# Performance work log

Hardware: AMD Instinct MI355X
Metric: run time of the kernel (lower is better)

The kernel has to match this reference:

```python
import jax, jax.numpy as jnp
import numpy as np

H, D_IN, D_Q, D_V = 8, 16, 32, 32
N = M = 4096


def setup_inputs() -> dict:
    key = jax.random.key(0)
    ks = jax.random.split(key, 12)
    s_in = 1.0 / np.sqrt(D_IN)
    s_fc = 1.0 / np.sqrt(H * D_V)
    return {
        "x": jax.random.normal(ks[0], (N, D_IN), jnp.float32),
        "y": jax.random.normal(ks[1], (M, D_IN), jnp.float32),
        # per-head stacked weights: [H, D_IN, D_Q/ D_V]
        "Wq": jax.random.uniform(ks[2], (H, D_IN, D_Q), jnp.float32, -s_in, s_in),
        "bq": jax.random.uniform(ks[3], (H, D_Q), jnp.float32, -s_in, s_in),
        "Wk": jax.random.uniform(ks[4], (H, D_IN, D_Q), jnp.float32, -s_in, s_in),
        "bk": jax.random.uniform(ks[5], (H, D_Q), jnp.float32, -s_in, s_in),
        "Wv": jax.random.uniform(ks[6], (H, D_IN, D_V), jnp.float32, -s_in, s_in),
        "bv": jax.random.uniform(ks[7], (H, D_V), jnp.float32, -s_in, s_in),
        "Wo": jax.random.uniform(ks[8], (H * D_V, D_IN), jnp.float32, -s_fc, s_fc),
        "bo": jax.random.uniform(ks[9], (D_IN,), jnp.float32, -s_fc, s_fc),
    }


def reference(x, y, Wq, bq, Wk, bk, Wv, bv, Wo, bo):
    # batched per-head projections (fuses the 8 tiny Linears of the torch loop)
    q = jnp.einsum("nd,hdq->hnq", x, Wq) + bq[:, None, :]   # [H, N, D_Q]
    k = jnp.einsum("md,hdq->hmq", y, Wk) + bk[:, None, :]   # [H, M, D_Q]
    v = jnp.einsum("md,hdv->hmv", y, Wv) + bv[:, None, :]   # [H, M, D_V]
    scores = jnp.einsum("hnq,hmq->hnm", q, k) / jnp.sqrt(jnp.float32(D_Q))
    attn = jax.nn.softmax(scores, axis=-1)                  # [H, N, M]
    heads = jnp.einsum("hnm,hmv->hnv", attn, v)             # [H, N, D_V]
    # torch.cat(head_outputs, dim=-1): head h occupies columns [h*D_V:(h+1)*D_V]
    concat = jnp.transpose(heads, (1, 0, 2)).reshape(x.shape[0], H * D_V)
    return concat @ Wo + bo                                  # [N, D_IN]
```

## Files before the change

### kernel.cpp

```cpp
#include <hip/hip_runtime.h>
#include <hip/hip_bf16.h>

typedef __attribute__((ext_vector_type(8))) short bf16x8;
typedef __attribute__((ext_vector_type(4))) float f32x4;
typedef unsigned short u16;
typedef unsigned int u32;

#define NH 8
#define NN 4096
#define MM 4096

__device__ __forceinline__ u16 f2bf(float f) {
  u32 b = __float_as_uint(f);
  b += 0x7FFFu + ((b >> 16) & 1u);
  return (u16)(b >> 16);
}

__device__ __forceinline__ u32 pack_rnu(float a, float b) {
  u32 ua = __float_as_uint(a) + 0x8000u;
  u32 ub = __float_as_uint(b) + 0x8000u;
#if __has_builtin(__builtin_amdgcn_perm)
  return __builtin_amdgcn_perm(ub, ua, 0x07060302u);
#else
  return (ua >> 16) | (ub & 0xFFFF0000u);
#endif
}

#if __has_builtin(__builtin_amdgcn_exp2f)
__device__ __forceinline__ float exp2_fast(float x) { return __builtin_amdgcn_exp2f(x); }
#else
__device__ __forceinline__ float exp2_fast(float x) { return __expf(x * 0.69314718055994531f); }
#endif

__global__ __launch_bounds__(256) void proj_kernel(
    const float* __restrict__ x, const float* __restrict__ y,
    const float* __restrict__ Wq, const float* __restrict__ bq,
    const float* __restrict__ Wk, const float* __restrict__ bk,
    const float* __restrict__ Wv, const float* __restrict__ bv,
    u16* __restrict__ qs, u16* __restrict__ ks, u16* __restrict__ vT)
{
  __shared__ u16 sv[256][33];
  const int bid = blockIdx.x;
  const int tid = threadIdx.x;
  if (bid < 256) {
    int idx = bid * 256 + tid;
    int t = idx >> 15;
    int h = (idx >> 12) & 7;
    int row = idx & 4095;
    const float* src = (t ? y : x) + row * 16;
    const float* W = (t ? Wk : Wq) + (h << 9);
    const float* b = (t ? bk : bq) + (h << 5);
    const float scale = t ? 1.0f : 0.25503635116465163f;
    float4 r4[4];
#pragma unroll
    for (int i = 0; i < 4; ++i) r4[i] = ((const float4*)src)[i];
    const float* r = (const float*)r4;
    u16* out = (t ? ks : qs) + (idx & 32767) * 32;
#pragma unroll
    for (int j = 0; j < 32; ++j) {
      float a = b[j];
#pragma unroll
      for (int i = 0; i < 16; ++i) a = fmaf(r[i], W[i * 32 + j], a);
      out[j] = f2bf(a * scale);
    }
  } else {
    int vb = bid - 256;
    int h = vb >> 4;
    int kb = (vb & 15) << 8;
    const float* src = y + (kb + tid) * 16;
    const float* W = Wv + (h << 9);
    const float* b = bv + (h << 5);
    float4 r4[4];
#pragma unroll
    for (int i = 0; i < 4; ++i) r4[i] = ((const float4*)src)[i];
    const float* r = (const float*)r4;
#pragma unroll
    for (int j = 0; j < 32; ++j) {
      float a = b[j];
#pragma unroll
      for (int i = 0; i < 16; ++i) a = fmaf(r[i], W[i * 32 + j], a);
      sv[tid][j] = f2bf(a);
    }
    __syncthreads();
    int dv = tid >> 3;
    int c = (tid & 7) << 5;
    u16* dst = vT + (((h << 5) + dv) << 12) + kb + c;
#pragma unroll
    for (int q = 0; q < 4; ++q) {
      uint4 w;
      w.x = (u32)sv[c + 4 * q + 0][dv]      | ((u32)sv[c + 4 * q + 1][dv] << 16);
      w.y = (u32)sv[c + 4 * q + 2][dv]      | ((u32)sv[c + 4 * q + 3][dv] << 16);
      w.z = (u32)sv[c + 16 + 4 * q + 0][dv] | ((u32)sv[c + 16 + 4 * q + 1][dv] << 16);
      w.w = (u32)sv[c + 16 + 4 * q + 2][dv] | ((u32)sv[c + 16 + 4 * q + 3][dv] << 16);
      *(uint4*)(dst + q * 8) = w;
    }
  }
}

#define KST 40
#define VST 72
#define VSZ (32 * VST)

__global__ __launch_bounds__(256) void flash_kernel(
    const u16* __restrict__ qs, const u16* __restrict__ ksrc,
    const u16* __restrict__ vT, float* __restrict__ accP,
    float* __restrict__ lsumP)
{
  __shared__ u16 sK[128 * KST];
  __shared__ u16 sVT[2 * VSZ];
  const int h = blockIdx.y;
  const int qt = blockIdx.x;
  const int z = blockIdx.z;
  const int nIter = (MM / 128) / gridDim.z;
  const int kb0 = z * (MM / gridDim.z);
  const int tid = threadIdx.x;
  const int wv = tid >> 6;
  const int lane = tid & 63;
  const int d = lane & 15;
  const int g = lane >> 4;
  const int qrowA = (qt << 7) + (wv << 5) + d;
  const int qrowB = qrowA + 16;

  union U4 { uint4 q; bf16x8 v; };
  U4 qfA, qfB;
  qfA.q = *(const uint4*)(qs + (((h << 12) + qrowA) << 5) + (g << 3));
  qfB.q = *(const uint4*)(qs + (((h << 12) + qrowB) << 5) + (g << 3));

  float lsA = 0.f, lsB = 0.f;
  f32x4 accA0 = {0.f, 0.f, 0.f, 0.f}, accA1 = {0.f, 0.f, 0.f, 0.f};
  f32x4 accB0 = {0.f, 0.f, 0.f, 0.f}, accB1 = {0.f, 0.f, 0.f, 0.f};
  const f32x4 zero = {0.f, 0.f, 0.f, 0.f};

  const u16* gK = ksrc + (h << 17) + (kb0 << 5) + ((tid >> 1) << 5) + ((tid & 1) << 4);
  const u16* gV = vT + (((h << 5) + (tid >> 3)) << 12) + kb0 + ((tid & 7) << 4);
  u16* wK = sK + (tid >> 1) * KST + ((tid & 1) << 4);
  u16* wV = sVT + ((tid & 7) >> 2) * VSZ + (tid >> 3) * VST + ((tid & 7) & 3) * 16;

  {
    uint4 a = *(const uint4*)gK, b = *(const uint4*)(gK + 8);
    uint4 c = *(const uint4*)gV, e = *(const uint4*)(gV + 8);
    *(uint4*)wK = a; *(uint4*)(wK + 8) = b;
    *(uint4*)wV = c; *(uint4*)(wV + 8) = e;
  }
  __syncthreads();

  auto compute = [&](const u16* kb, const u16* vb) {
    U4 kf[4];
#pragma unroll
    for (int t = 0; t < 4; ++t)
      kf[t].q = *(const uint4*)(kb + (t * 16 + d) * KST + (g << 3));

    union { u32 w[4]; bf16x8 v; } pbA0, pbA1, pbB0, pbB1;
    {
      f32x4 s0, s1, s2, s3;
      s0 = __builtin_amdgcn_mfma_f32_16x16x32_bf16(kf[0].v, qfA.v, zero, 0, 0, 0);
      s1 = __builtin_amdgcn_mfma_f32_16x16x32_bf16(kf[1].v, qfA.v, zero, 0, 0, 0);
      s2 = __builtin_amdgcn_mfma_f32_16x16x32_bf16(kf[2].v, qfA.v, zero, 0, 0, 0);
      s3 = __builtin_amdgcn_mfma_f32_16x16x32_bf16(kf[3].v, qfA.v, zero, 0, 0, 0);
      float e[16];
      e[0]=exp2_fast(s0.x); e[1]=exp2_fast(s0.y); e[2]=exp2_fast(s0.z); e[3]=exp2_fast(s0.w);
      e[4]=exp2_fast(s1.x); e[5]=exp2_fast(s1.y); e[6]=exp2_fast(s1.z); e[7]=exp2_fast(s1.w);
      e[8]=exp2_fast(s2.x); e[9]=exp2_fast(s2.y); e[10]=exp2_fast(s2.z); e[11]=exp2_fast(s2.w);
      e[12]=exp2_fast(s3.x); e[13]=exp2_fast(s3.y); e[14]=exp2_fast(s3.z); e[15]=exp2_fast(s3.w);
      lsA += ((e[0]+e[1])+(e[2]+e[3])) + ((e[4]+e[5])+(e[6]+e[7]))
           + ((e[8]+e[9])+(e[10]+e[11])) + ((e[12]+e[13])+(e[14]+e[15]));
      pbA0.w[0] = pack_rnu(e[0], e[1]);   pbA0.w[1] = pack_rnu(e[2], e[3]);
      pbA0.w[2] = pack_rnu(e[4], e[5]);   pbA0.w[3] = pack_rnu(e[6], e[7]);
      pbA1.w[0] = pack_rnu(e[8], e[9]);   pbA1.w[1] = pack_rnu(e[10], e[11]);
      pbA1.w[2] = pack_rnu(e[12], e[13]); pbA1.w[3] = pack_rnu(e[14], e[15]);
    }
    {
      f32x4 s0, s1, s2, s3;
      s0 = __builtin_amdgcn_mfma_f32_16x16x32_bf16(kf[0].v, qfB.v, zero, 0, 0, 0);
      s1 = __builtin_amdgcn_mfma_f32_16x16x32_bf16(kf[1].v, qfB.v, zero, 0, 0, 0);
      s2 = __builtin_amdgcn_mfma_f32_16x16x32_bf16(kf[2].v, qfB.v, zero, 0, 0, 0);
      s3 = __builtin_amdgcn_mfma_f32_16x16x32_bf16(kf[3].v, qfB.v, zero, 0, 0, 0);
      float e[16];
      e[0]=exp2_fast(s0.x); e[1]=exp2_fast(s0.y); e[2]=exp2_fast(s0.z); e[3]=exp2_fast(s0.w);
      e[4]=exp2_fast(s1.x); e[5]=exp2_fast(s1.y); e[6]=exp2_fast(s1.z); e[7]=exp2_fast(s1.w);
      e[8]=exp2_fast(s2.x); e[9]=exp2_fast(s2.y); e[10]=exp2_fast(s2.z); e[11]=exp2_fast(s2.w);
      e[12]=exp2_fast(s3.x); e[13]=exp2_fast(s3.y); e[14]=exp2_fast(s3.z); e[15]=exp2_fast(s3.w);
      lsB += ((e[0]+e[1])+(e[2]+e[3])) + ((e[4]+e[5])+(e[6]+e[7]))
           + ((e[8]+e[9])+(e[10]+e[11])) + ((e[12]+e[13])+(e[14]+e[15]));
      pbB0.w[0] = pack_rnu(e[0], e[1]);   pbB0.w[1] = pack_rnu(e[2], e[3]);
      pbB0.w[2] = pack_rnu(e[4], e[5]);   pbB0.w[3] = pack_rnu(e[6], e[7]);
      pbB1.w[0] = pack_rnu(e[8], e[9]);   pbB1.w[1] = pack_rnu(e[10], e[11]);
      pbB1.w[2] = pack_rnu(e[12], e[13]); pbB1.w[3] = pack_rnu(e[14], e[15]);
    }
    U4 vf0, vf1, vf2, vf3;
    const u16* vp = vb + d * VST;
    vf0.q = *(const uint4*)(vp + (g << 3));
    vf1.q = *(const uint4*)(vp + 32 + (g << 3));
    vp += 16 * VST;
    vf2.q = *(const uint4*)(vp + (g << 3));
    vf3.q = *(const uint4*)(vp + 32 + (g << 3));
    accA0 = __builtin_amdgcn_mfma_f32_16x16x32_bf16(vf0.v, pbA0.v, accA0, 0, 0, 0);
    accA0 = __builtin_amdgcn_mfma_f32_16x16x32_bf16(vf1.v, pbA1.v, accA0, 0, 0, 0);
    accA1 = __builtin_amdgcn_mfma_f32_16x16x32_bf16(vf2.v, pbA0.v, accA1, 0, 0, 0);
    accA1 = __builtin_amdgcn_mfma_f32_16x16x32_bf16(vf3.v, pbA1.v, accA1, 0, 0, 0);
    accB0 = __builtin_amdgcn_mfma_f32_16x16x32_bf16(vf0.v, pbB0.v, accB0, 0, 0, 0);
    accB0 = __builtin_amdgcn_mfma_f32_16x16x32_bf16(vf1.v, pbB1.v, accB0, 0, 0, 0);
    accB1 = __builtin_amdgcn_mfma_f32_16x16x32_bf16(vf2.v, pbB0.v, accB1, 0, 0, 0);
    accB1 = __builtin_amdgcn_mfma_f32_16x16x32_bf16(vf3.v, pbB1.v, accB1, 0, 0, 0);
  };

#pragma unroll 1
  for (int it = 0; it < nIter; ++it) {
    uint4 a, b, c, e;
    if (it < nIter - 1) {
      gK += 4096; gV += 128;
      a = *(const uint4*)gK; b = *(const uint4*)(gK + 8);
      c = *(const uint4*)gV; e = *(const uint4*)(gV + 8);
    }
    compute(sK, sVT);
    compute(sK + 64 * KST, sVT + VSZ);
    __syncthreads();
    if (it < nIter - 1) {
      *(uint4*)wK = a; *(uint4*)(wK + 8) = b;
      *(uint4*)wV = c; *(uint4*)(wV + 8) = e;
      __syncthreads();
    }
  }

  lsA += __shfl_xor(lsA, 16);
  lsA += __shfl_xor(lsA, 32);
  lsB += __shfl_xor(lsB, 16);
  lsB += __shfl_xor(lsB, 32);
  if (g == 0) {
    lsumP[((z * NH + h) << 12) + qrowA] = lsA;
    lsumP[((z * NH + h) << 12) + qrowB] = lsB;
  }
  float* cpA = accP + z * (NN * 256) + (qrowA << 8) + (h << 5) + (g << 2);
  *(float4*)cpA        = make_float4(accA0.x, accA0.y, accA0.z, accA0.w);
  *(float4*)(cpA + 16) = make_float4(accA1.x, accA1.y, accA1.z, accA1.w);
  float* cpB = accP + z * (NN * 256) + (qrowB << 8) + (h << 5) + (g << 2);
  *(float4*)cpB        = make_float4(accB0.x, accB0.y, accB0.z, accB0.w);
  *(float4*)(cpB + 16) = make_float4(accB1.x, accB1.y, accB1.z, accB1.w);
}

__global__ __launch_bounds__(256) void combine_kernel(
    const float* __restrict__ accP, const float* __restrict__ lsumP,
    float* __restrict__ concat, int S)
{
  int idx = blockIdx.x * 256 + threadIdx.x;
  int n = idx >> 8;
  int h = (idx & 255) >> 5;
  float o = 0.f, l = 0.f;
  for (int s = 0; s < S; ++s) {
    o += accP[s * (NN * 256) + idx];
    l += lsumP[((s * NH + h) << 12) + n];
  }
  concat[idx] = o / l;
}

__global__ __launch_bounds__(256) void out_gemm_kernel(
    const float* __restrict__ concat, const float* __restrict__ Wo,
    const float* __restrict__ bo, float* __restrict__ out)
{
  __shared__ float sWo[4096];
  int tid = threadIdx.x;
  for (int i = tid; i < 4096; i += 256) sWo[i] = Wo[i];
  __syncthreads();
  int idx = blockIdx.x * 256 + tid;
  int n = idx >> 4;
  int c = idx & 15;
  const float4* crow = (const float4*)(concat + (n << 8));
  float a = bo[c];
#pragma unroll 4
  for (int i4 = 0; i4 < 64; ++i4) {
    float4 cv = crow[i4];
    a = fmaf(cv.x, sWo[(i4 * 4 + 0) * 16 + c], a);
    a = fmaf(cv.y, sWo[(i4 * 4 + 1) * 16 + c], a);
    a = fmaf(cv.z, sWo[(i4 * 4 + 2) * 16 + c], a);
    a = fmaf(cv.w, sWo[(i4 * 4 + 3) * 16 + c], a);
  }
  out[idx] = a;
}

extern "C" void kernel_launch(void* const* d_in, const int* in_sizes, int n_in,
                              void* d_out, int out_size, void* d_ws, size_t ws_size,
                              hipStream_t stream) {
  const float* x  = (const float*)d_in[0];
  const float* y  = (const float*)d_in[1];
  const float* Wq = (const float*)d_in[2];
  const float* bq = (const float*)d_in[3];
  const float* Wk = (const float*)d_in[4];
  const float* bk = (const float*)d_in[5];
  const float* Wv = (const float*)d_in[6];
  const float* bv = (const float*)d_in[7];
  const float* Wo = (const float*)d_in[8];
  const float* bo = (const float*)d_in[9];
  float* out = (float*)d_out;

  u16* qs = (u16*)d_ws;
  u16* ks = qs + (NH * NN * 32);
  u16* vT = ks + (NH * MM * 32);
  float* concat = (float*)(vT + (NH * MM * 32));
  float* accP = concat;
  const int S = (ws_size >= (size_t)(6 + 16) * 1024 * 1024 + 512 * 1024) ? 4 : 1;
  float* lsumP = accP + (size_t)S * (NN * 256);

  hipLaunchKernelGGL(proj_kernel, dim3(384), dim3(256), 0, stream,
                     x, y, Wq, bq, Wk, bk, Wv, bv, qs, ks, vT);
  hipLaunchKernelGGL(flash_kernel, dim3(32, NH, S), dim3(256), 0, stream,
                     qs, ks, vT, accP, lsumP);
  hipLaunchKernelGGL(combine_kernel, dim3(4096), dim3(256), 0, stream,
                     accP, lsumP, concat, S);
  hipLaunchKernelGGL(out_gemm_kernel, dim3(256), dim3(256), 0, stream, concat, Wo, bo, out);
}
```

Before: 61.88 us.

## Compute softmax row sums via MFMA and fuse combine with output GEMM

The per-element VALU adds that built the softmax denominator are replaced by extra MFMA ops that multiply the bf16 probability fragments by a ones vector, so the denominator comes out of the matrix unit. The separate combine and output-projection kernels are merged into one kernel that reduces the split partials into shared memory and then applies Wo with a split-K reduction. This removes one launch and the concat round trip through global memory. The trade-offs are that the row sums now use bf16-rounded probabilities, there are four more MFMAs per tile, and the fused kernel does a small amount of work per block.

```diff
diff --git a/kernel.cpp b/kernel.cpp
--- a/kernel.cpp
+++ b/kernel.cpp
@@ -126,9 +126,15 @@
   qfA.q = *(const uint4*)(qs + (((h << 12) + qrowA) << 5) + (g << 3));
   qfB.q = *(const uint4*)(qs + (((h << 12) + qrowB) << 5) + (g << 3));
 
-  float lsA = 0.f, lsB = 0.f;
+  union { u32 w[4]; bf16x8 v; } ones;
+  {
+    u32 ow = (d == 0) ? 0x3F803F80u : 0u;
+    ones.w[0] = ow; ones.w[1] = ow; ones.w[2] = ow; ones.w[3] = ow;
+  }
+
   f32x4 accA0 = {0.f, 0.f, 0.f, 0.f}, accA1 = {0.f, 0.f, 0.f, 0.f};
   f32x4 accB0 = {0.f, 0.f, 0.f, 0.f}, accB1 = {0.f, 0.f, 0.f, 0.f};
+  f32x4 accLA = {0.f, 0.f, 0.f, 0.f}, accLB = {0.f, 0.f, 0.f, 0.f};
   const f32x4 zero = {0.f, 0.f, 0.f, 0.f};
 
   const u16* gK = ksrc + (h << 17) + (kb0 << 5) + ((tid >> 1) << 5) + ((tid & 1) << 4);
@@ -162,8 +168,6 @@
       e[4]=exp2_fast(s1.x); e[5]=exp2_fast(s1.y); e[6]=exp2_fast(s1.z); e[7]=exp2_fast(s1.w);
       e[8]=exp2_fast(s2.x); e[9]=exp2_fast(s2.y); e[10]=exp2_fast(s2.z); e[11]=exp2_fast(s2.w);
       e[12]=exp2_fast(s3.x); e[13]=exp2_fast(s3.y); e[14]=exp2_fast(s3.z); e[15]=exp2_fast(s3.w);
-      lsA += ((e[0]+e[1])+(e[2]+e[3])) + ((e[4]+e[5])+(e[6]+e[7]))
-           + ((e[8]+e[9])+(e[10]+e[11])) + ((e[12]+e[13])+(e[14]+e[15]));
       pbA0.w[0] = pack_rnu(e[0], e[1]);   pbA0.w[1] = pack_rnu(e[2], e[3]);
       pbA0.w[2] = pack_rnu(e[4], e[5]);   pbA0.w[3] = pack_rnu(e[6], e[7]);
       pbA1.w[0] = pack_rnu(e[8], e[9]);   pbA1.w[1] = pack_rnu(e[10], e[11]);
@@ -180,13 +184,15 @@
       e[4]=exp2_fast(s1.x); e[5]=exp2_fast(s1.y); e[6]=exp2_fast(s1.z); e[7]=exp2_fast(s1.w);
       e[8]=exp2_fast(s2.x); e[9]=exp2_fast(s2.y); e[10]=exp2_fast(s2.z); e[11]=exp2_fast(s2.w);
       e[12]=exp2_fast(s3.x); e[13]=exp2_fast(s3.y); e[14]=exp2_fast(s3.z); e[15]=exp2_fast(s3.w);
-      lsB += ((e[0]+e[1])+(e[2]+e[3])) + ((e[4]+e[5])+(e[6]+e[7]))
-           + ((e[8]+e[9])+(e[10]+e[11])) + ((e[12]+e[13])+(e[14]+e[15]));
       pbB0.w[0] = pack_rnu(e[0], e[1]);   pbB0.w[1] = pack_rnu(e[2], e[3]);
       pbB0.w[2] = pack_rnu(e[4], e[5]);   pbB0.w[3] = pack_rnu(e[6], e[7]);
       pbB1.w[0] = pack_rnu(e[8], e[9]);   pbB1.w[1] = pack_rnu(e[10], e[11]);
       pbB1.w[2] = pack_rnu(e[12], e[13]); pbB1.w[3] = pack_rnu(e[14], e[15]);
     }
+    accLA = __builtin_amdgcn_mfma_f32_16x16x32_bf16(ones.v, pbA0.v, accLA, 0, 0, 0);
+    accLA = __builtin_amdgcn_mfma_f32_16x16x32_bf16(ones.v, pbA1.v, accLA, 0, 0, 0);
+    accLB = __builtin_amdgcn_mfma_f32_16x16x32_bf16(ones.v, pbB0.v, accLB, 0, 0, 0);
+    accLB = __builtin_amdgcn_mfma_f32_16x16x32_bf16(ones.v, pbB1.v, accLB, 0, 0, 0);
     U4 vf0, vf1, vf2, vf3;
     const u16* vp = vb + d * VST;
     vf0.q = *(const uint4*)(vp + (g << 3));
@@ -222,13 +228,9 @@
     }
   }
 
-  lsA += __shfl_xor(lsA, 16);
-  lsA += __shfl_xor(lsA, 32);
-  lsB += __shfl_xor(lsB, 16);
-  lsB += __shfl_xor(lsB, 32);
   if (g == 0) {
-    lsumP[((z * NH + h) << 12) + qrowA] = lsA;
-    lsumP[((z * NH + h) << 12) + qrowB] = lsB;
+    lsumP[((z * NH + h) << 12) + qrowA] = accLA.x;
+    lsumP[((z * NH + h) << 12) + qrowB] = accLB.x;
   }
   float* cpA = accP + z * (NN * 256) + (qrowA << 8) + (h << 5) + (g << 2);
   *(float4*)cpA        = make_float4(accA0.x, accA0.y, accA0.z, accA0.w);
@@ -238,43 +240,51 @@
   *(float4*)(cpB + 16) = make_float4(accB1.x, accB1.y, accB1.z, accB1.w);
 }
 
-__global__ __launch_bounds__(256) void combine_kernel(
+__global__ __launch_bounds__(256) void out_fused_kernel(
     const float* __restrict__ accP, const float* __restrict__ lsumP,
-    float* __restrict__ concat, int S)
+    const float* __restrict__ Wo, const float* __restrict__ bo,
+    float* __restrict__ out, int S)
 {
-  int idx = blockIdx.x * 256 + threadIdx.x;
-  int n = idx >> 8;
-  int h = (idx & 255) >> 5;
-  float o = 0.f, l = 0.f;
-  for (int s = 0; s < S; ++s) {
-    o += accP[s * (NN * 256) + idx];
-    l += lsumP[((s * NH + h) << 12) + n];
-  }
-  concat[idx] = o / l;
-}
-
-__global__ __launch_bounds__(256) void out_gemm_kernel(
-    const float* __restrict__ concat, const float* __restrict__ Wo,
-    const float* __restrict__ bo, float* __restrict__ out)
-{
-  __shared__ float sWo[4096];
-  int tid = threadIdx.x;
-  for (int i = tid; i < 4096; i += 256) sWo[i] = Wo[i];
+  __shared__ float cn[4][256];
+  __shared__ float sQ[4][4][16];
+  const int tid = threadIdx.x;
+  const int n0 = blockIdx.x << 2;
+
+  {
+    const int r = tid >> 6, u = tid & 63;
+    const int n = n0 + r;
+    float4 o = make_float4(0.f, 0.f, 0.f, 0.f);
+    for (int s = 0; s < S; ++s) {
+      const float4 v = *(const float4*)(accP + (size_t)s * (NN * 256) + (n << 8) + (u << 2));
+      o.x += v.x; o.y += v.y; o.z += v.z; o.w += v.w;
+    }
+    const int hh = u >> 3;
+    float l = 0.f;
+    for (int s = 0; s < S; ++s) l += lsumP[((s * NH + hh) << 12) + n];
+    const float inv = 1.0f / l;
+    *(float4*)&cn[r][u << 2] = make_float4(o.x * inv, o.y * inv, o.z * inv, o.w * inv);
+  }
   __syncthreads();
-  int idx = blockIdx.x * 256 + tid;
-  int n = idx >> 4;
-  int c = idx & 15;
-  const float4* crow = (const float4*)(concat + (n << 8));
-  float a = bo[c];
-#pragma unroll 4
-  for (int i4 = 0; i4 < 64; ++i4) {
-    float4 cv = crow[i4];
-    a = fmaf(cv.x, sWo[(i4 * 4 + 0) * 16 + c], a);
-    a = fmaf(cv.y, sWo[(i4 * 4 + 1) * 16 + c], a);
-    a = fmaf(cv.z, sWo[(i4 * 4 + 2) * 16 + c], a);
-    a = fmaf(cv.w, sWo[(i4 * 4 + 3) * 16 + c], a);
-  }
-  out[idx] = a;
+
+  {
+    const int r = tid >> 6, ks = (tid >> 4) & 3, c = tid & 15;
+    const float* cr = &cn[r][ks << 6];
+    const float* wp = Wo + (ks << 6) * 16 + c;
+    float a = 0.f;
+#pragma unroll
+    for (int jj = 0; jj < 64; ++jj) {
+      const int j2 = (jj + (ks << 4)) & 63;
+      a = fmaf(cr[j2], wp[j2 * 16], a);
+    }
+    sQ[r][ks][c] = a;
+  }
+  __syncthreads();
+
+  if (tid < 64) {
+    const int r = tid >> 4, c = tid & 15;
+    float v = bo[c] + ((sQ[r][0][c] + sQ[r][1][c]) + (sQ[r][2][c] + sQ[r][3][c]));
+    out[((n0 + r) << 4) + c] = v;
+  }
 }
 
 extern "C" void kernel_launch(void* const* d_in, const int* in_sizes, int n_in,
@@ -295,8 +305,7 @@
   u16* qs = (u16*)d_ws;
   u16* ks = qs + (NH * NN * 32);
   u16* vT = ks + (NH * MM * 32);
-  float* concat = (float*)(vT + (NH * MM * 32));
-  float* accP = concat;
+  float* accP = (float*)(vT + (NH * MM * 32));
   const int S = (ws_size >= (size_t)(6 + 16) * 1024 * 1024 + 512 * 1024) ? 4 : 1;
   float* lsumP = accP + (size_t)S * (NN * 256);
 
@@ -304,7 +313,6 @@
                      x, y, Wq, bq, Wk, bk, Wv, bv, qs, ks, vT);
   hipLaunchKernelGGL(flash_kernel, dim3(32, NH, S), dim3(256), 0, stream,
                      qs, ks, vT, accP, lsumP);
-  hipLaunchKernelGGL(combine_kernel, dim3(4096), dim3(256), 0, stream,
-                     accP, lsumP, concat, S);
-  hipLaunchKernelGGL(out_gemm_kernel, dim3(256), dim3(256), 0, stream, concat, Wo, bo, out);
-}
+  hipLaunchKernelGGL(out_fused_kernel, dim3(1024), dim3(256), 0, stream,
+                     accP, lsumP, Wo, bo, out, S);
+}
```

Result: no change. 62.45 us (+0.9%).
